# Kernel tuning notes

Measured on AMD Instinct MI355X. Metric: run time of the kernel, lower is better.

## Reference

```python
import jax, jax.numpy as jnp
import numpy as np

OUT_F, IN_F = 11008, 4096
GROUP = 64                      # group_size, axis=0 grouping
G = OUT_F * IN_F // GROUP       # number of groups = 704512


def setup_inputs() -> dict:
    key = jax.random.key(0)
    ks = jax.random.split(key, 7)
    x = jax.random.normal(ks[0], (512, IN_F), dtype=jnp.float32)
    # packed 4-bit weights: two nibbles per byte, packed along the group axis
    W_q = jax.random.randint(ks[1], (GROUP // 2, G), 0, 256, dtype=jnp.int32)
    # per-group dequant params (scale = 1/quant_scale in the torch code)
    scale = jax.random.uniform(ks[2], (1, G), dtype=jnp.float32) * 0.01 + 1e-4
    zero = jax.random.uniform(ks[3], (1, G), dtype=jnp.float32) * 15.0
    # low-rank correction (LoRC): W_eff = W_dq + U @ V
    U = jax.random.normal(ks[4], (OUT_F, 32), dtype=jnp.float32) * 0.02
    V = jax.random.normal(ks[5], (32, IN_F), dtype=jnp.float32) * 0.02
    bias = jax.random.normal(ks[6], (OUT_F,), dtype=jnp.float32)
    return {"x": x, "W_q": W_q, "scale": scale, "zero": zero,
            "U": U, "V": V, "bias": bias}


def _dequantize(W_q, scale, zero):
    # unpack_4bit_u8: high nibble -> first half of rows, low nibble -> second half
    hi = ((W_q >> 4) & 0xF).astype(jnp.float32)   # [32, G]
    lo = (W_q & 0xF).astype(jnp.float32)          # [32, G]
    Wg = jnp.concatenate([hi, lo], axis=0)        # [64, G] = [group_size, G]
    W = (Wg - zero) * scale                       # per-group affine dequant
    return W.reshape(OUT_F, IN_F)


def reference(x, W_q, scale, zero, U, V, bias):
    W = _dequantize(W_q, scale, zero)             # [out, in]
    W = W + U @ V                                 # low-rank correction
    # nn.Linear semantics: out = x @ W.T + bias
    return x @ W.T + bias
```

## Files before the change

kernel.cpp:

```cpp
#include <hip/hip_runtime.h>
#include <cstdint>

typedef short  s16x8 __attribute__((ext_vector_type(8)));
typedef float  f32x4 __attribute__((ext_vector_type(4)));
typedef int    i32x4 __attribute__((ext_vector_type(4)));
typedef int    i32x2 __attribute__((ext_vector_type(2)));
typedef unsigned short u16x4 __attribute__((ext_vector_type(4)));

#define OUT_F 11008
#define IN_F  4096
#define MROWS 512
#define GQ4   176128
#define HALF  5504
#define RMOD  172

__device__ __forceinline__ unsigned short f2bf(float f) {
  unsigned u = __builtin_bit_cast(unsigned, f);
  return (unsigned short)((u + 0x8000u) >> 16);
}
__device__ __forceinline__ float bfbits(unsigned bits) {
  return __builtin_bit_cast(float, bits);
}
__device__ __forceinline__ unsigned cvtpk(float a, float b) {
  unsigned r;
  asm("v_cvt_pk_bf16_f32 %0, %1, %2" : "=v"(r) : "v"(a), "v"(b));
  return r;
}

__global__ __launch_bounds__(256) void convert_k(const float* __restrict__ x,
                                                 const float* __restrict__ U,
                                                 unsigned short* __restrict__ xbf,
                                                 unsigned short* __restrict__ Ubf) {
  int i = blockIdx.x * 256 + threadIdx.x;
  const int NX = (MROWS * IN_F) / 4;
  const int NU = (OUT_F * 32) / 4;
  if (i >= NX + NU) return;
  const float* src; unsigned short* dst; int idx;
  if (i < NX) { src = x; dst = xbf; idx = i; }
  else        { src = U; dst = Ubf; idx = i - NX; }
  f32x4 v = *(const f32x4*)(src + (size_t)idx * 4);
  u16x4 o;
  o[0] = f2bf(v[0]); o[1] = f2bf(v[1]); o[2] = f2bf(v[2]); o[3] = f2bf(v[3]);
  *(u16x4*)(dst + (size_t)idx * 4) = o;
}

__global__ __launch_bounds__(256) void mz_k(const float* __restrict__ scale,
                                            const float* __restrict__ zero,
                                            f32x4* __restrict__ mz) {
  int idx = blockIdx.x * 256 + threadIdx.x;
  if (idx >= 176128) return;
  f32x4 s = *(const f32x4*)(scale + (size_t)idx * 4);
  f32x4 z = *(const f32x4*)(zero  + (size_t)idx * 4);
  f32x4 m;
#pragma unroll
  for (int e = 0; e < 4; ++e) m[e] = -(z[e] + 128.f) * s[e];
  mz[idx] = m;
}

__global__ __launch_bounds__(256) void pcalc_k(const float* __restrict__ x,
                                               const float* __restrict__ V,
                                               float* __restrict__ P) {
  int m  = (blockIdx.x >> 3) * 8 + (threadIdx.x >> 5);
  int j  = threadIdx.x & 31;
  int k0 = (blockIdx.x & 7) * 512;
  const float* xr = x + (size_t)m * IN_F + k0;
  const float* vr = V + (size_t)j * IN_F + k0;
  float a = 0.f;
#pragma unroll 4
  for (int k = 0; k < 512; k += 4) {
    f32x4 xv = *(const f32x4*)(xr + k);
    f32x4 vv = *(const f32x4*)(vr + k);
    a += xv[0]*vv[0] + xv[1]*vv[1] + xv[2]*vv[2] + xv[3]*vv[3];
  }
  atomicAdd(P + m * 32 + j, a);
}

__global__ __launch_bounds__(256) void wdeq_k(const i32x4* __restrict__ Wq4,
                                              const float* __restrict__ scale,
                                              const float* __restrict__ zero,
                                              unsigned short* __restrict__ Wbf) {
  int n  = blockIdx.x * 256 + threadIdx.x;
  int jo = n / 88064;
  int ch = n - jo * 88064;
  int r  = ch >> 9;
  const int chL = ch & 511;
  const int cc0 = ch * 8;
  f32x4 s0 = *(const f32x4*)(scale + cc0);
  f32x4 s1 = *(const f32x4*)(scale + cc0 + 4);
  f32x4 z0 = *(const f32x4*)(zero + cc0);
  f32x4 z1 = *(const f32x4*)(zero + cc0 + 4);
  float sv[8], mzv[8];
#pragma unroll
  for (int e = 0; e < 4; ++e) {
    sv[e]      = s0[e]; mzv[e]     = -(z0[e] + 128.f) * s0[e];
    sv[e + 4]  = s1[e]; mzv[e + 4] = -(z1[e] + 128.f) * s1[e];
  }
#pragma unroll
  for (int jj = 0; jj < 8; ++jj) {
    int j = jo * 8 + jj;
    i32x4 w0 = Wq4[(size_t)j * GQ4 + ch * 2];
    i32x4 w1 = Wq4[(size_t)j * GQ4 + ch * 2 + 1];
    float h[8], l[8];
#pragma unroll
    for (int e = 0; e < 8; ++e) {
      int v = (e < 4) ? w0[e] : w1[e - 4];
      float qh = bfbits(0x43000000u | (((unsigned)v & 0xF0u) << 12));
      float ql = bfbits(0x43000000u | (((unsigned)v & 0x0Fu) << 16));
      h[e] = __builtin_fmaf(qh, sv[e], mzv[e]);
      l[e] = __builtin_fmaf(ql, sv[e], mzv[e]);
    }
    i32x4 hh = { (int)cvtpk(h[0], h[1]), (int)cvtpk(h[2], h[3]),
                 (int)cvtpk(h[4], h[5]), (int)cvtpk(h[6], h[7]) };
    i32x4 ll = { (int)cvtpk(l[0], l[1]), (int)cvtpk(l[2], l[3]),
                 (int)cvtpk(l[4], l[5]), (int)cvtpk(l[6], l[7]) };
    int o  = j * RMOD + r;
    int o2 = o + HALF;
    unsigned sc  = ((unsigned)chL & ~7u) | (((unsigned)chL ^ (unsigned)o)  & 7u);
    unsigned sc2 = ((unsigned)chL & ~7u) | (((unsigned)chL ^ (unsigned)o2) & 7u);
    *(i32x4*)(Wbf + (size_t)o  * IN_F + sc  * 8) = hh;
    *(i32x4*)(Wbf + (size_t)o2 * IN_F + sc2 * 8) = ll;
  }
}

__global__ __launch_bounds__(512, 6) void gemm_fast(
    const unsigned short* __restrict__ xbf,
    const unsigned short* __restrict__ Wbf,
    const float*          __restrict__ Pf,
    const i32x4*          __restrict__ Ubf4,
    const float*          __restrict__ bias,
    float*                __restrict__ out)
{
  extern __shared__ __align__(16) unsigned short smem[];

  const int tid  = threadIdx.x;
  const int lane = tid & 63;
  const int wid  = tid >> 6;
  const int wm   = wid >> 2;
  const int wn   = wid & 3;

  const int b  = blockIdx.x;
  const int L  = (b & 7) * 86 + (b >> 3);
  const int gn = L >> 3;
  const int gm = L & 7;
  const int m0 = gm * 64;
  const int o0 = gn * 128;

  const int arow = tid >> 3;
  const unsigned a_src = (unsigned)(m0 + arow) * IN_F +
                         (((tid & 7) ^ (arow & 7)) * 8);
  size_t b_src[2];
#pragma unroll
  for (int it = 0; it < 2; ++it)
    b_src[it] = (size_t)(o0 + it * 64 + (tid >> 3)) * IN_F + (tid & 7) * 8;

  const int akey   = (lane & 7) << 3;
  const int a_base = (wm * 32 + (lane & 15)) * 64 + ((lane >> 4) * 8);
  const int b_base = (wn * 32 + (lane & 15)) * 64 + ((lane >> 4) * 8);

  f32x4 acc[2][2];
  {
    f32x4 zf = {0.f, 0.f, 0.f, 0.f};
#pragma unroll
    for (int i = 0; i < 2; ++i)
#pragma unroll
      for (int j = 0; j < 2; ++j) acc[i][j] = zf;
  }
  f32x4 pf0, pf1; i32x4 uuF;

  auto issueA = [&](int buf, int k0s) {
    unsigned short* Adst = smem + buf * 4096;
    __builtin_amdgcn_global_load_lds(
        (const __attribute__((address_space(1))) unsigned int*)(xbf + a_src + k0s),
        (__attribute__((address_space(3))) unsigned int*)(Adst + tid * 8),
        16, 0, 0);
  };
  auto issueB = [&](int buf, int k0s) {
    unsigned short* Bdst = smem + 8192 + buf * 8192;
#pragma unroll
    for (int it = 0; it < 2; ++it) {
      __builtin_amdgcn_global_load_lds(
          (const __attribute__((address_space(1))) unsigned int*)(Wbf + b_src[it] + k0s),
          (__attribute__((address_space(3))) unsigned int*)(Bdst + it * 4096 + tid * 8),
          16, 0, 0);
    }
  };
  auto compute = [&](int buf) {
    const unsigned short* Ac = smem + buf * 4096;
    const unsigned short* Bc = smem + 8192 + buf * 8192;
    __builtin_amdgcn_s_setprio(1);
#pragma unroll
    for (int kk = 0; kk < 64; kk += 32) {
      s16x8 av[2], bv[2];
#pragma unroll
      for (int f = 0; f < 2; ++f)
        av[f] = *(const s16x8*)(Ac + ((a_base + f * 1024 + kk) ^ akey));
#pragma unroll
      for (int f = 0; f < 2; ++f)
        bv[f] = *(const s16x8*)(Bc + ((b_base + f * 1024 + kk) ^ akey));
#pragma unroll
      for (int i = 0; i < 2; ++i)
#pragma unroll
        for (int j = 0; j < 2; ++j)
          acc[i][j] = __builtin_amdgcn_mfma_f32_16x16x32_bf16(av[i], bv[j], acc[i][j], 0, 0, 0);
    }
    __builtin_amdgcn_s_setprio(0);
  };
  auto loadF = [&]() {
    int row = tid >> 3, h8 = tid & 7;
    if (h8 < 4) {
      pf0 = *(const f32x4*)(Pf + (m0 + row) * 32 + h8 * 8);
      pf1 = *(const f32x4*)(Pf + (m0 + row) * 32 + h8 * 8 + 4);
    }
    int rw = tid >> 2, h4 = tid & 3;
    uuF = Ubf4[(size_t)(o0 + rw) * 4 + h4];
  };
  auto writeF = [&](int buf) {
    unsigned short* An = smem + buf * 4096;
    unsigned short* Bn = smem + 8192 + buf * 8192;
    i32x4 zi = {0, 0, 0, 0};
    {
      int row = tid >> 3, h8 = tid & 7, key = row & 7;
      i32x4 v = zi;
      if (h8 < 4)
        v = i32x4{ (int)cvtpk(pf0[0], pf0[1]), (int)cvtpk(pf0[2], pf0[3]),
                   (int)cvtpk(pf1[0], pf1[1]), (int)cvtpk(pf1[2], pf1[3]) };
      *(i32x4*)(An + row * 64 + ((h8 ^ key) * 8)) = v;
    }
    {
      int rw = tid >> 2, h4 = tid & 3, key = rw & 7;
      *(i32x4*)(Bn + rw * 64 + ((h4 ^ key) * 8))       = uuF;
      *(i32x4*)(Bn + rw * 64 + (((h4 + 4) ^ key) * 8)) = zi;
    }
  };

  issueA(0, 0);
  issueB(0, 0);
  __syncthreads();

  for (int t = 0; t < 63; ++t) {
    int cur = t & 1, nxt = cur ^ 1;
    issueA(nxt, (t + 1) * 64);
    issueB(nxt, (t + 1) * 64);
    compute(cur);
    __syncthreads();
  }
  loadF();
  compute(1);
  writeF(0);
  __syncthreads();
  compute(0);

#pragma unroll
  for (int fn = 0; fn < 2; ++fn) {
    int o = o0 + wn * 32 + fn * 16 + (lane & 15);
    float bv = bias[o];
#pragma unroll
    for (int fm = 0; fm < 2; ++fm) {
      int m = m0 + wm * 32 + fm * 16 + ((lane >> 4) << 2);
#pragma unroll
      for (int j = 0; j < 4; ++j)
        out[(size_t)(m + j) * OUT_F + o] = acc[fm][fn][j] + bv;
    }
  }
}

__global__ __launch_bounds__(512, 6) void milo_gemm(
    const unsigned short* __restrict__ xbf,
    const i32x4*          __restrict__ Wq4,
    const f32x4*          __restrict__ Sc4,
    const f32x4*          __restrict__ Mz4,
    const float*          __restrict__ Pf,
    const i32x4*          __restrict__ Ubf4,
    const float*          __restrict__ bias,
    float*                __restrict__ out)
{
  extern __shared__ __align__(16) unsigned short smem[];
  const int tid  = threadIdx.x;
  const int lane = tid & 63;
  const int wid  = tid >> 6;
  const int wm   = wid >> 1;
  const int wn   = wid & 1;
  const int b  = blockIdx.x;
  const int L  = (b & 7) * 86 + (b >> 3);
  const int gn = L >> 2;
  const int gm = L & 3;
  const int m0 = gm * 128;
  const int o0 = gn * 32;
  const int tr = tid >> 4;
  unsigned wq_off, sc_off;
  {
    int o = o0 + tr;
    int g = o / RMOD;
    int r = o - g * RMOD;
    wq_off = (unsigned)g * GQ4 + (unsigned)r * 1024u + (tid & 15);
    sc_off = (unsigned)r * 1024u + (tid & 15);
  }
  unsigned a_src[2];
#pragma unroll
  for (int it = 0; it < 2; ++it) {
    int row   = wid * 16 + it * 8 + (lane >> 3);
    int chunk = (lane & 7) ^ (lane >> 3);
    a_src[it] = (unsigned)(m0 + row) * IN_F + chunk * 8;
  }
  const int akey   = (lane & 7) << 3;
  const int a_base = (wm * 32 + (lane & 15)) * 64 + ((lane >> 4) * 8);
  const int b_base = (wn * 32 + (lane & 15)) * 64 + ((lane >> 4) * 8);
  f32x4 acc[2][2];
  {
    f32x4 zf = {0.f, 0.f, 0.f, 0.f};
#pragma unroll
    for (int i = 0; i < 2; ++i)
#pragma unroll
      for (int j = 0; j < 2; ++j) acc[i][j] = zf;
  }
  i32x4 wq; f32x4 s4, mz4;
  f32x4 pf[2]; i32x4 uuF;
  auto issueA = [&](int buf, int k0s) {
    unsigned short* Adst = smem + buf * 8192;
#pragma unroll
    for (int it = 0; it < 2; ++it) {
      __builtin_amdgcn_global_load_lds(
          (const __attribute__((address_space(1))) unsigned int*)(xbf + a_src[it] + k0s),
          (__attribute__((address_space(3))) unsigned int*)(Adst + (wid * 16 + it * 8) * 64),
          16, 0, 0);
    }
  };
  auto loadB = [&](int kq) {
    wq  = Wq4[wq_off + kq];
    s4  = Sc4[sc_off + kq];
    mz4 = Mz4[sc_off + kq];
  };
  auto writeB = [&](int buf) {
    unsigned short* Bn = smem + 16384 + buf * 4096;
    int scol = ((tid & 15) * 4) ^ ((tr & 7) << 3);
    float h[4], l[4];
#pragma unroll
    for (int e = 0; e < 4; ++e) {
      int v = wq[e];
      float qh = bfbits(0x43000000u | (((unsigned)v & 0xF0u) << 12));
      float ql = bfbits(0x43000000u | (((unsigned)v & 0x0Fu) << 16));
      h[e] = __builtin_fmaf(qh, s4[e], mz4[e]);
      l[e] = __builtin_fmaf(ql, s4[e], mz4[e]);
    }
    i32x2 hh = { (int)cvtpk(h[0], h[1]), (int)cvtpk(h[2], h[3]) };
    i32x2 ll = { (int)cvtpk(l[0], l[1]), (int)cvtpk(l[2], l[3]) };
    *(i32x2*)(Bn + tr * 64 + scol)        = hh;
    *(i32x2*)(Bn + (tr + 32) * 64 + scol) = ll;
  };
  auto loadF = [&]() {
    int row = tid >> 2, h4 = tid & 3;
#pragma unroll
    for (int q = 0; q < 2; ++q)
      pf[q] = *(const f32x4*)(Pf + (m0 + row) * 32 + h4 * 8 + q * 4);
    int rw = tid >> 3, h8 = tid & 7;
    int oc = (rw < 32) ? (o0 + rw) : (HALF + o0 + rw - 32);
    uuF = Ubf4[oc * 4 + (h8 & 3)];
  };
  auto writeF = [&](int buf) {
    unsigned short* An = smem + buf * 8192;
    unsigned short* Bn = smem + 16384 + buf * 4096;
    i32x4 zi = {0, 0, 0, 0};
    {
      int row = tid >> 2, h4 = tid & 3;
      int key = (row & 7) << 3;
      i32x4 t4 = { (int)cvtpk(pf[0][0], pf[0][1]), (int)cvtpk(pf[0][2], pf[0][3]),
                   (int)cvtpk(pf[1][0], pf[1][1]), (int)cvtpk(pf[1][2], pf[1][3]) };
      *(i32x4*)(An + row * 64 + ((h4 * 8) ^ key))      = t4;
      *(i32x4*)(An + row * 64 + ((32 + h4 * 8) ^ key)) = zi;
    }
    {
      int rw = tid >> 3, h8 = tid & 7;
      int key = (rw & 7) << 3;
      *(i32x4*)(Bn + rw * 64 + ((h8 * 8) ^ key)) = (h8 < 4) ? uuF : zi;
    }
  };
  auto compute = [&](int buf) {
    const unsigned short* Ac = smem + buf * 8192;
    const unsigned short* Bc = smem + 16384 + buf * 4096;
    __builtin_amdgcn_s_setprio(1);
#pragma unroll
    for (int kk = 0; kk < 64; kk += 32) {
      s16x8 av[2], bv[2];
#pragma unroll
      for (int f = 0; f < 2; ++f)
        av[f] = *(const s16x8*)(Ac + ((a_base + f * 1024 + kk) ^ akey));
#pragma unroll
      for (int f = 0; f < 2; ++f)
        bv[f] = *(const s16x8*)(Bc + ((b_base + f * 1024 + kk) ^ akey));
#pragma unroll
      for (int i = 0; i < 2; ++i)
#pragma unroll
        for (int j = 0; j < 2; ++j)
          acc[i][j] = __builtin_amdgcn_mfma_f32_16x16x32_bf16(av[i], bv[j], acc[i][j], 0, 0, 0);
    }
    __builtin_amdgcn_s_setprio(0);
  };
  loadB(0);
  issueA(0, 0);
  writeB(0);
  __syncthreads();
  for (int t = 0; t < 63; ++t) {
    int cur = t & 1, nxt = cur ^ 1;
    loadB((t + 1) * 16);
    issueA(nxt, (t + 1) * 64);
    compute(cur);
    writeB(nxt);
    __syncthreads();
  }
  loadF();
  compute(1);
  writeF(0);
  __syncthreads();
  compute(0);
#pragma unroll
  for (int fn = 0; fn < 2; ++fn) {
    int c = wn * 32 + fn * 16 + (lane & 15);
    int o = (c < 32) ? (o0 + c) : (HALF + o0 + (c - 32));
    float bv = bias[o];
#pragma unroll
    for (int fm = 0; fm < 2; ++fm) {
      int m = m0 + wm * 32 + fm * 16 + ((lane >> 4) << 2);
#pragma unroll
      for (int j = 0; j < 4; ++j)
        out[(size_t)(m + j) * OUT_F + o] = acc[fm][fn][j] + bv;
    }
  }
}

extern "C" void kernel_launch(void* const* d_in, const int* in_sizes, int n_in,
                              void* d_out, int out_size, void* d_ws, size_t ws_size,
                              hipStream_t stream) {
  const float* x     = (const float*)d_in[0];
  const int*   Wq    = (const int*)d_in[1];
  const float* scale = (const float*)d_in[2];
  const float* zero  = (const float*)d_in[3];
  const float* U     = (const float*)d_in[4];
  const float* V     = (const float*)d_in[5];
  const float* bias  = (const float*)d_in[6];
  float* out = (float*)d_out;

  unsigned short* xbf = (unsigned short*)d_ws;
  unsigned short* Ubf = xbf + (size_t)MROWS * IN_F;
  float*          P   = (float*)(Ubf + (size_t)OUT_F * 32);
  char*           rest = (char*)(P + (size_t)MROWS * 32);
  const size_t base   = (size_t)MROWS * IN_F * 2 + (size_t)OUT_F * 32 * 2
                      + (size_t)MROWS * 32 * 4;
  const size_t wbf_sz = (size_t)OUT_F * IN_F * 2;

  (void)hipMemsetAsync(P, 0, (size_t)MROWS * 32 * sizeof(float), stream);
  convert_k<<<2392, 256, 0, stream>>>(x, U, xbf, Ubf);
  pcalc_k<<<512, 256, 0, stream>>>(x, V, P);

  if (ws_size >= base + wbf_sz) {
    unsigned short* Wbf = (unsigned short*)rest;
    wdeq_k<<<1376, 256, 0, stream>>>((const i32x4*)Wq, scale, zero, Wbf);
    gemm_fast<<<688, 512, 49152, stream>>>(xbf, Wbf, P, (const i32x4*)Ubf,
                                           bias, out);
  } else {
    float* mz = (float*)rest;
    mz_k<<<688, 256, 0, stream>>>(scale, zero, (f32x4*)mz);
    milo_gemm<<<688, 512, 49152, stream>>>(xbf, (const i32x4*)Wq,
                                           (const f32x4*)scale, (const f32x4*)mz,
                                           P, (const i32x4*)Ubf, bias, out);
  }
}
```

Baseline: 137.3 us.

## Double GEMM M-tile to 128 rows and flatten dequant kernel parallelism

The bf16 GEMM block tile grows from 64x128 to 128x128. Each wave now holds 4x2 MFMA accumulators, the grid halves to 344 blocks, shared memory rises to 64 KB, and launch bounds drop to 4 blocks per CU. The goal is to cut redundant W tile reloads from global memory by reusing each B tile across more rows of x. The dequant kernel also drops its 8-iteration loop over j and launches 8x more threads, one output chunk each, for more parallelism in exchange for reloading scale and zero once per thread. The trade-off is that 344 blocks may underfill the GPU's CUs and the larger tile raises register pressure.

```diff
diff --git a/kernel.cpp b/kernel.cpp
--- a/kernel.cpp
+++ b/kernel.cpp
@@ -79,50 +79,43 @@
                                               const float* __restrict__ scale,
                                               const float* __restrict__ zero,
                                               unsigned short* __restrict__ Wbf) {
-  int n  = blockIdx.x * 256 + threadIdx.x;
-  int jo = n / 88064;
-  int ch = n - jo * 88064;
-  int r  = ch >> 9;
-  const int chL = ch & 511;
+  int n   = blockIdx.x * 256 + threadIdx.x;
+  int j   = n / 88064;
+  int ch  = n - j * 88064;
+  int r   = ch >> 9;
+  int chL = ch & 511;
   const int cc0 = ch * 8;
   f32x4 s0 = *(const f32x4*)(scale + cc0);
   f32x4 s1 = *(const f32x4*)(scale + cc0 + 4);
   f32x4 z0 = *(const f32x4*)(zero + cc0);
   f32x4 z1 = *(const f32x4*)(zero + cc0 + 4);
-  float sv[8], mzv[8];
-#pragma unroll
-  for (int e = 0; e < 4; ++e) {
-    sv[e]      = s0[e]; mzv[e]     = -(z0[e] + 128.f) * s0[e];
-    sv[e + 4]  = s1[e]; mzv[e + 4] = -(z1[e] + 128.f) * s1[e];
-  }
-#pragma unroll
-  for (int jj = 0; jj < 8; ++jj) {
-    int j = jo * 8 + jj;
-    i32x4 w0 = Wq4[(size_t)j * GQ4 + ch * 2];
-    i32x4 w1 = Wq4[(size_t)j * GQ4 + ch * 2 + 1];
-    float h[8], l[8];
-#pragma unroll
-    for (int e = 0; e < 8; ++e) {
-      int v = (e < 4) ? w0[e] : w1[e - 4];
-      float qh = bfbits(0x43000000u | (((unsigned)v & 0xF0u) << 12));
-      float ql = bfbits(0x43000000u | (((unsigned)v & 0x0Fu) << 16));
-      h[e] = __builtin_fmaf(qh, sv[e], mzv[e]);
-      l[e] = __builtin_fmaf(ql, sv[e], mzv[e]);
-    }
-    i32x4 hh = { (int)cvtpk(h[0], h[1]), (int)cvtpk(h[2], h[3]),
-                 (int)cvtpk(h[4], h[5]), (int)cvtpk(h[6], h[7]) };
-    i32x4 ll = { (int)cvtpk(l[0], l[1]), (int)cvtpk(l[2], l[3]),
-                 (int)cvtpk(l[4], l[5]), (int)cvtpk(l[6], l[7]) };
-    int o  = j * RMOD + r;
-    int o2 = o + HALF;
-    unsigned sc  = ((unsigned)chL & ~7u) | (((unsigned)chL ^ (unsigned)o)  & 7u);
-    unsigned sc2 = ((unsigned)chL & ~7u) | (((unsigned)chL ^ (unsigned)o2) & 7u);
-    *(i32x4*)(Wbf + (size_t)o  * IN_F + sc  * 8) = hh;
-    *(i32x4*)(Wbf + (size_t)o2 * IN_F + sc2 * 8) = ll;
-  }
-}
-
-__global__ __launch_bounds__(512, 6) void gemm_fast(
+  i32x4 w0 = Wq4[(size_t)j * GQ4 + ch * 2];
+  i32x4 w1 = Wq4[(size_t)j * GQ4 + ch * 2 + 1];
+  float h[8], l[8];
+#pragma unroll
+  for (int e = 0; e < 8; ++e) {
+    int   v = (e < 4) ? w0[e] : w1[e - 4];
+    float s = (e < 4) ? s0[e] : s1[e - 4];
+    float z = (e < 4) ? z0[e] : z1[e - 4];
+    float m = -(z + 128.f) * s;
+    float qh = bfbits(0x43000000u | (((unsigned)v & 0xF0u) << 12));
+    float ql = bfbits(0x43000000u | (((unsigned)v & 0x0Fu) << 16));
+    h[e] = __builtin_fmaf(qh, s, m);
+    l[e] = __builtin_fmaf(ql, s, m);
+  }
+  i32x4 hh = { (int)cvtpk(h[0], h[1]), (int)cvtpk(h[2], h[3]),
+               (int)cvtpk(h[4], h[5]), (int)cvtpk(h[6], h[7]) };
+  i32x4 ll = { (int)cvtpk(l[0], l[1]), (int)cvtpk(l[2], l[3]),
+               (int)cvtpk(l[4], l[5]), (int)cvtpk(l[6], l[7]) };
+  int o  = j * RMOD + r;
+  int o2 = o + HALF;
+  unsigned sc  = ((unsigned)chL & ~7u) | (((unsigned)chL ^ (unsigned)o)  & 7u);
+  unsigned sc2 = ((unsigned)chL & ~7u) | (((unsigned)chL ^ (unsigned)o2) & 7u);
+  *(i32x4*)(Wbf + (size_t)o  * IN_F + sc  * 8) = hh;
+  *(i32x4*)(Wbf + (size_t)o2 * IN_F + sc2 * 8) = ll;
+}
+
+__global__ __launch_bounds__(512, 4) void gemm_fast(
     const unsigned short* __restrict__ xbf,
     const unsigned short* __restrict__ Wbf,
     const float*          __restrict__ Pf,
@@ -139,43 +132,48 @@
   const int wn   = wid & 3;
 
   const int b  = blockIdx.x;
-  const int L  = (b & 7) * 86 + (b >> 3);
-  const int gn = L >> 3;
-  const int gm = L & 7;
-  const int m0 = gm * 64;
+  const int L  = (b & 7) * 43 + (b >> 3);
+  const int gn = L >> 2;
+  const int gm = L & 3;
+  const int m0 = gm * 128;
   const int o0 = gn * 128;
 
-  const int arow = tid >> 3;
-  const unsigned a_src = (unsigned)(m0 + arow) * IN_F +
-                         (((tid & 7) ^ (arow & 7)) * 8);
+  unsigned a_src[2];
+#pragma unroll
+  for (int it = 0; it < 2; ++it)
+    a_src[it] = (unsigned)(m0 + it * 64 + (tid >> 3)) * IN_F +
+                (((tid & 7) ^ ((tid >> 3) & 7)) * 8);
   size_t b_src[2];
 #pragma unroll
   for (int it = 0; it < 2; ++it)
     b_src[it] = (size_t)(o0 + it * 64 + (tid >> 3)) * IN_F + (tid & 7) * 8;
 
   const int akey   = (lane & 7) << 3;
-  const int a_base = (wm * 32 + (lane & 15)) * 64 + ((lane >> 4) * 8);
+  const int a_base = (wm * 64 + (lane & 15)) * 64 + ((lane >> 4) * 8);
   const int b_base = (wn * 32 + (lane & 15)) * 64 + ((lane >> 4) * 8);
 
-  f32x4 acc[2][2];
+  f32x4 acc[4][2];
   {
     f32x4 zf = {0.f, 0.f, 0.f, 0.f};
 #pragma unroll
-    for (int i = 0; i < 2; ++i)
+    for (int i = 0; i < 4; ++i)
 #pragma unroll
       for (int j = 0; j < 2; ++j) acc[i][j] = zf;
   }
   f32x4 pf0, pf1; i32x4 uuF;
 
   auto issueA = [&](int buf, int k0s) {
-    unsigned short* Adst = smem + buf * 4096;
-    __builtin_amdgcn_global_load_lds(
-        (const __attribute__((address_space(1))) unsigned int*)(xbf + a_src + k0s),
-        (__attribute__((address_space(3))) unsigned int*)(Adst + tid * 8),
-        16, 0, 0);
+    unsigned short* Adst = smem + buf * 8192;
+#pragma unroll
+    for (int it = 0; it < 2; ++it) {
+      __builtin_amdgcn_global_load_lds(
+          (const __attribute__((address_space(1))) unsigned int*)(xbf + a_src[it] + k0s),
+          (__attribute__((address_space(3))) unsigned int*)(Adst + it * 4096 + tid * 8),
+          16, 0, 0);
+    }
   };
   auto issueB = [&](int buf, int k0s) {
-    unsigned short* Bdst = smem + 8192 + buf * 8192;
+    unsigned short* Bdst = smem + 16384 + buf * 8192;
 #pragma unroll
     for (int it = 0; it < 2; ++it) {
       __builtin_amdgcn_global_load_lds(
@@ -185,20 +183,20 @@
     }
   };
   auto compute = [&](int buf) {
-    const unsigned short* Ac = smem + buf * 4096;
-    const unsigned short* Bc = smem + 8192 + buf * 8192;
+    const unsigned short* Ac = smem + buf * 8192;
+    const unsigned short* Bc = smem + 16384 + buf * 8192;
     __builtin_amdgcn_s_setprio(1);
 #pragma unroll
     for (int kk = 0; kk < 64; kk += 32) {
-      s16x8 av[2], bv[2];
-#pragma unroll
-      for (int f = 0; f < 2; ++f)
+      s16x8 av[4], bv[2];
+#pragma unroll
+      for (int f = 0; f < 4; ++f)
         av[f] = *(const s16x8*)(Ac + ((a_base + f * 1024 + kk) ^ akey));
 #pragma unroll
       for (int f = 0; f < 2; ++f)
         bv[f] = *(const s16x8*)(Bc + ((b_base + f * 1024 + kk) ^ akey));
 #pragma unroll
-      for (int i = 0; i < 2; ++i)
+      for (int i = 0; i < 4; ++i)
 #pragma unroll
         for (int j = 0; j < 2; ++j)
           acc[i][j] = __builtin_amdgcn_mfma_f32_16x16x32_bf16(av[i], bv[j], acc[i][j], 0, 0, 0);
@@ -206,31 +204,22 @@
     __builtin_amdgcn_s_setprio(0);
   };
   auto loadF = [&]() {
-    int row = tid >> 3, h8 = tid & 7;
-    if (h8 < 4) {
-      pf0 = *(const f32x4*)(Pf + (m0 + row) * 32 + h8 * 8);
-      pf1 = *(const f32x4*)(Pf + (m0 + row) * 32 + h8 * 8 + 4);
-    }
-    int rw = tid >> 2, h4 = tid & 3;
-    uuF = Ubf4[(size_t)(o0 + rw) * 4 + h4];
+    int row = tid >> 2, h4 = tid & 3;
+    pf0 = *(const f32x4*)(Pf + (m0 + row) * 32 + h4 * 8);
+    pf1 = *(const f32x4*)(Pf + (m0 + row) * 32 + h4 * 8 + 4);
+    uuF = Ubf4[(size_t)(o0 + row) * 4 + h4];
   };
   auto writeF = [&](int buf) {
-    unsigned short* An = smem + buf * 4096;
-    unsigned short* Bn = smem + 8192 + buf * 8192;
+    unsigned short* An = smem + buf * 8192;
+    unsigned short* Bn = smem + 16384 + buf * 8192;
     i32x4 zi = {0, 0, 0, 0};
-    {
-      int row = tid >> 3, h8 = tid & 7, key = row & 7;
-      i32x4 v = zi;
-      if (h8 < 4)
-        v = i32x4{ (int)cvtpk(pf0[0], pf0[1]), (int)cvtpk(pf0[2], pf0[3]),
-                   (int)cvtpk(pf1[0], pf1[1]), (int)cvtpk(pf1[2], pf1[3]) };
-      *(i32x4*)(An + row * 64 + ((h8 ^ key) * 8)) = v;
-    }
-    {
-      int rw = tid >> 2, h4 = tid & 3, key = rw & 7;
-      *(i32x4*)(Bn + rw * 64 + ((h4 ^ key) * 8))       = uuF;
-      *(i32x4*)(Bn + rw * 64 + (((h4 + 4) ^ key) * 8)) = zi;
-    }
+    int row = tid >> 2, h4 = tid & 3, key = row & 7;
+    i32x4 t4 = { (int)cvtpk(pf0[0], pf0[1]), (int)cvtpk(pf0[2], pf0[3]),
+                 (int)cvtpk(pf1[0], pf1[1]), (int)cvtpk(pf1[2], pf1[3]) };
+    *(i32x4*)(An + row * 64 + ((h4 ^ key) * 8))       = t4;
+    *(i32x4*)(An + row * 64 + (((h4 + 4) ^ key) * 8)) = zi;
+    *(i32x4*)(Bn + row * 64 + ((h4 ^ key) * 8))       = uuF;
+    *(i32x4*)(Bn + row * 64 + (((h4 + 4) ^ key) * 8)) = zi;
   };
 
   issueA(0, 0);
@@ -255,8 +244,8 @@
     int o = o0 + wn * 32 + fn * 16 + (lane & 15);
     float bv = bias[o];
 #pragma unroll
-    for (int fm = 0; fm < 2; ++fm) {
-      int m = m0 + wm * 32 + fm * 16 + ((lane >> 4) << 2);
+    for (int fm = 0; fm < 4; ++fm) {
+      int m = m0 + wm * 64 + fm * 16 + ((lane >> 4) << 2);
 #pragma unroll
       for (int j = 0; j < 4; ++j)
         out[(size_t)(m + j) * OUT_F + o] = acc[fm][fn][j] + bv;
@@ -453,8 +442,8 @@
 
   if (ws_size >= base + wbf_sz) {
     unsigned short* Wbf = (unsigned short*)rest;
-    wdeq_k<<<1376, 256, 0, stream>>>((const i32x4*)Wq, scale, zero, Wbf);
-    gemm_fast<<<688, 512, 49152, stream>>>(xbf, Wbf, P, (const i32x4*)Ubf,
+    wdeq_k<<<11008, 256, 0, stream>>>((const i32x4*)Wq, scale, zero, Wbf);
+    gemm_fast<<<344, 512, 65536, stream>>>(xbf, Wbf, P, (const i32x4*)Ubf,
                                            bias, out);
   } else {
     float* mz = (float*)rest;
```

New measurement: 132.5 us. -3.5%, faster.

## Fuse prep kernels into one launch and triple-buffer the bf16 GEMM pipeline

Applied to the files above, without the earlier changes.

Merges the weight dequantization, x/U bf16 conversion and x@V projection into a single prep kernel, with one 4-bit group slice per thread instead of eight per thread. This removes two launches and lets the three preprocessing jobs overlap on the device. The GEMM switches from double to triple buffering in LDS, using explicit vmcnt waits and raw barriers so loads run two stages ahead. LDS per block grows to 72KB and the occupancy hint drops from 6 to 4, which may reduce the number of resident blocks.

```diff
diff --git a/kernel.cpp b/kernel.cpp
--- a/kernel.cpp
+++ b/kernel.cpp
@@ -25,6 +25,237 @@
   unsigned r;
   asm("v_cvt_pk_bf16_f32 %0, %1, %2" : "=v"(r) : "v"(a), "v"(b));
   return r;
+}
+
+__global__ __launch_bounds__(256) void prep_k(const float* __restrict__ x,
+                                              const float* __restrict__ U,
+                                              const float* __restrict__ scale,
+                                              const float* __restrict__ zero,
+                                              const float* __restrict__ V,
+                                              const i32x4* __restrict__ Wq4,
+                                              unsigned short* __restrict__ xbf,
+                                              unsigned short* __restrict__ Ubf,
+                                              float* __restrict__ P,
+                                              unsigned short* __restrict__ Wbf) {
+  const int blk = blockIdx.x;
+  const int tid = threadIdx.x;
+  if (blk < 11008) {
+    int n   = blk * 256 + tid;
+    int j   = n / 88064;
+    int ch  = n - j * 88064;
+    int r   = ch >> 9;
+    int chL = ch & 511;
+    const int cc0 = ch * 8;
+    f32x4 s0 = *(const f32x4*)(scale + cc0);
+    f32x4 s1 = *(const f32x4*)(scale + cc0 + 4);
+    f32x4 z0 = *(const f32x4*)(zero + cc0);
+    f32x4 z1 = *(const f32x4*)(zero + cc0 + 4);
+    i32x4 w0 = Wq4[(size_t)j * GQ4 + ch * 2];
+    i32x4 w1 = Wq4[(size_t)j * GQ4 + ch * 2 + 1];
+    float h[8], l[8];
+#pragma unroll
+    for (int e = 0; e < 8; ++e) {
+      int   v = (e < 4) ? w0[e] : w1[e - 4];
+      float s = (e < 4) ? s0[e] : s1[e - 4];
+      float z = (e < 4) ? z0[e] : z1[e - 4];
+      float m = -(z + 128.f) * s;
+      float qh = bfbits(0x43000000u | (((unsigned)v & 0xF0u) << 12));
+      float ql = bfbits(0x43000000u | (((unsigned)v & 0x0Fu) << 16));
+      h[e] = __builtin_fmaf(qh, s, m);
+      l[e] = __builtin_fmaf(ql, s, m);
+    }
+    i32x4 hh = { (int)cvtpk(h[0], h[1]), (int)cvtpk(h[2], h[3]),
+                 (int)cvtpk(h[4], h[5]), (int)cvtpk(h[6], h[7]) };
+    i32x4 ll = { (int)cvtpk(l[0], l[1]), (int)cvtpk(l[2], l[3]),
+                 (int)cvtpk(l[4], l[5]), (int)cvtpk(l[6], l[7]) };
+    int o  = j * RMOD + r;
+    int o2 = o + HALF;
+    unsigned sc  = ((unsigned)chL & ~7u) | (((unsigned)chL ^ (unsigned)o)  & 7u);
+    unsigned sc2 = ((unsigned)chL & ~7u) | (((unsigned)chL ^ (unsigned)o2) & 7u);
+    *(i32x4*)(Wbf + (size_t)o  * IN_F + sc  * 8) = hh;
+    *(i32x4*)(Wbf + (size_t)o2 * IN_F + sc2 * 8) = ll;
+  } else if (blk < 13400) {
+    int i = (blk - 11008) * 256 + tid;
+    const int NX = (MROWS * IN_F) / 4;
+    const int NU = (OUT_F * 32) / 4;
+    if (i >= NX + NU) return;
+    const float* src; unsigned short* dst; int idx;
+    if (i < NX) { src = x; dst = xbf; idx = i; }
+    else        { src = U; dst = Ubf; idx = i - NX; }
+    f32x4 v = *(const f32x4*)(src + (size_t)idx * 4);
+    u16x4 o;
+    o[0] = f2bf(v[0]); o[1] = f2bf(v[1]); o[2] = f2bf(v[2]); o[3] = f2bf(v[3]);
+    *(u16x4*)(dst + (size_t)idx * 4) = o;
+  } else {
+    int bp = blk - 13400;
+    int m  = (bp >> 3) * 8 + (tid >> 5);
+    int j  = tid & 31;
+    int k0 = (bp & 7) * 512;
+    const float* xr = x + (size_t)m * IN_F + k0;
+    const float* vr = V + (size_t)j * IN_F + k0;
+    float a = 0.f;
+#pragma unroll 4
+    for (int k = 0; k < 512; k += 4) {
+      f32x4 xv = *(const f32x4*)(xr + k);
+      f32x4 vv = *(const f32x4*)(vr + k);
+      a += xv[0]*vv[0] + xv[1]*vv[1] + xv[2]*vv[2] + xv[3]*vv[3];
+    }
+    atomicAdd(P + m * 32 + j, a);
+  }
+}
+
+__global__ __launch_bounds__(512, 4) void gemm_fast(
+    const unsigned short* __restrict__ xbf,
+    const unsigned short* __restrict__ Wbf,
+    const float*          __restrict__ Pf,
+    const i32x4*          __restrict__ Ubf4,
+    const float*          __restrict__ bias,
+    float*                __restrict__ out)
+{
+  extern __shared__ __align__(16) unsigned short smem[];
+
+  const int tid  = threadIdx.x;
+  const int lane = tid & 63;
+  const int wid  = tid >> 6;
+  const int wm   = wid >> 2;
+  const int wn   = wid & 3;
+
+  const int b  = blockIdx.x;
+  const int L  = (b & 7) * 86 + (b >> 3);
+  const int gn = L >> 3;
+  const int gm = L & 7;
+  const int m0 = gm * 64;
+  const int o0 = gn * 128;
+
+  const int arow = tid >> 3;
+  const unsigned a_src = (unsigned)(m0 + arow) * IN_F +
+                         (((tid & 7) ^ (arow & 7)) * 8);
+  size_t b_src[2];
+#pragma unroll
+  for (int it = 0; it < 2; ++it)
+    b_src[it] = (size_t)(o0 + it * 64 + (tid >> 3)) * IN_F + (tid & 7) * 8;
+
+  const int akey   = (lane & 7) << 3;
+  const int a_base = (wm * 32 + (lane & 15)) * 64 + ((lane >> 4) * 8);
+  const int b_base = (wn * 32 + (lane & 15)) * 64 + ((lane >> 4) * 8);
+
+  f32x4 acc[2][2];
+  {
+    f32x4 zf = {0.f, 0.f, 0.f, 0.f};
+#pragma unroll
+    for (int i = 0; i < 2; ++i)
+#pragma unroll
+      for (int j = 0; j < 2; ++j) acc[i][j] = zf;
+  }
+  f32x4 pf0, pf1; i32x4 uuF;
+
+  auto issueT = [&](int ring, int k0s) {
+    unsigned short* Adst = smem + ring * 4096;
+    unsigned short* Bdst = smem + 12288 + ring * 8192;
+    __builtin_amdgcn_global_load_lds(
+        (const __attribute__((address_space(1))) unsigned int*)(xbf + a_src + k0s),
+        (__attribute__((address_space(3))) unsigned int*)(Adst + tid * 8),
+        16, 0, 0);
+#pragma unroll
+    for (int it = 0; it < 2; ++it) {
+      __builtin_amdgcn_global_load_lds(
+          (const __attribute__((address_space(1))) unsigned int*)(Wbf + b_src[it] + k0s),
+          (__attribute__((address_space(3))) unsigned int*)(Bdst + it * 4096 + tid * 8),
+          16, 0, 0);
+    }
+  };
+  auto compute = [&](int ring) {
+    const unsigned short* Ac = smem + ring * 4096;
+    const unsigned short* Bc = smem + 12288 + ring * 8192;
+    __builtin_amdgcn_s_setprio(1);
+#pragma unroll
+    for (int kk = 0; kk < 64; kk += 32) {
+      s16x8 av[2], bv[2];
+#pragma unroll
+      for (int f = 0; f < 2; ++f)
+        av[f] = *(const s16x8*)(Ac + ((a_base + f * 1024 + kk) ^ akey));
+#pragma unroll
+      for (int f = 0; f < 2; ++f)
+        bv[f] = *(const s16x8*)(Bc + ((b_base + f * 1024 + kk) ^ akey));
+#pragma unroll
+      for (int i = 0; i < 2; ++i)
+#pragma unroll
+        for (int j = 0; j < 2; ++j)
+          acc[i][j] = __builtin_amdgcn_mfma_f32_16x16x32_bf16(av[i], bv[j], acc[i][j], 0, 0, 0);
+    }
+    __builtin_amdgcn_s_setprio(0);
+  };
+  auto loadF = [&]() {
+    int row = tid >> 3, h8 = tid & 7;
+    if (h8 < 4) {
+      pf0 = *(const f32x4*)(Pf + (m0 + row) * 32 + h8 * 8);
+      pf1 = *(const f32x4*)(Pf + (m0 + row) * 32 + h8 * 8 + 4);
+    }
+    int rw = tid >> 2, h4 = tid & 3;
+    uuF = Ubf4[(size_t)(o0 + rw) * 4 + h4];
+  };
+  auto writeF = [&](int ring) {
+    unsigned short* An = smem + ring * 4096;
+    unsigned short* Bn = smem + 12288 + ring * 8192;
+    i32x4 zi = {0, 0, 0, 0};
+    {
+      int row = tid >> 3, h8 = tid & 7, key = row & 7;
+      i32x4 v = zi;
+      if (h8 < 4)
+        v = i32x4{ (int)cvtpk(pf0[0], pf0[1]), (int)cvtpk(pf0[2], pf0[3]),
+                   (int)cvtpk(pf1[0], pf1[1]), (int)cvtpk(pf1[2], pf1[3]) };
+      *(i32x4*)(An + row * 64 + ((h8 ^ key) * 8)) = v;
+    }
+    {
+      int rw = tid >> 2, h4 = tid & 3, key = rw & 7;
+      *(i32x4*)(Bn + rw * 64 + ((h4 ^ key) * 8))       = uuF;
+      *(i32x4*)(Bn + rw * 64 + (((h4 + 4) ^ key) * 8)) = zi;
+    }
+  };
+
+#define WAIT_LGKM0 asm volatile("s_waitcnt lgkmcnt(0)" ::: "memory")
+#define WAIT_VM(N) asm volatile("s_waitcnt vmcnt(" #N ")" ::: "memory")
+#define BAR        __builtin_amdgcn_s_barrier()
+
+  issueT(0, 0);
+  issueT(1, 64);
+  WAIT_VM(3);
+  BAR;
+
+#define STEP(RB, TI, IB) \
+  issueT(IB, (TI) * 64); compute(RB); WAIT_LGKM0; WAIT_VM(3); BAR;
+
+  for (int t3 = 0; t3 < 60; t3 += 3) {
+    STEP(0, t3 + 2, 2)
+    STEP(1, t3 + 3, 0)
+    STEP(2, t3 + 4, 1)
+  }
+  STEP(0, 62, 2)
+  STEP(1, 63, 0)
+  compute(2); WAIT_LGKM0; WAIT_VM(0); BAR;
+  loadF();
+  compute(0);
+  writeF(1);
+  WAIT_LGKM0; BAR;
+  compute(1);
+
+#undef STEP
+#undef WAIT_LGKM0
+#undef WAIT_VM
+#undef BAR
+
+#pragma unroll
+  for (int fn = 0; fn < 2; ++fn) {
+    int o = o0 + wn * 32 + fn * 16 + (lane & 15);
+    float bv = bias[o];
+#pragma unroll
+    for (int fm = 0; fm < 2; ++fm) {
+      int m = m0 + wm * 32 + fm * 16 + ((lane >> 4) << 2);
+#pragma unroll
+      for (int j = 0; j < 4; ++j)
+        out[(size_t)(m + j) * OUT_F + o] = acc[fm][fn][j] + bv;
+    }
+  }
 }
 
 __global__ __launch_bounds__(256) void convert_k(const float* __restrict__ x,
@@ -73,195 +304,6 @@
     a += xv[0]*vv[0] + xv[1]*vv[1] + xv[2]*vv[2] + xv[3]*vv[3];
   }
   atomicAdd(P + m * 32 + j, a);
-}
-
-__global__ __launch_bounds__(256) void wdeq_k(const i32x4* __restrict__ Wq4,
-                                              const float* __restrict__ scale,
-                                              const float* __restrict__ zero,
-                                              unsigned short* __restrict__ Wbf) {
-  int n  = blockIdx.x * 256 + threadIdx.x;
-  int jo = n / 88064;
-  int ch = n - jo * 88064;
-  int r  = ch >> 9;
-  const int chL = ch & 511;
-  const int cc0 = ch * 8;
-  f32x4 s0 = *(const f32x4*)(scale + cc0);
-  f32x4 s1 = *(const f32x4*)(scale + cc0 + 4);
-  f32x4 z0 = *(const f32x4*)(zero + cc0);
-  f32x4 z1 = *(const f32x4*)(zero + cc0 + 4);
-  float sv[8], mzv[8];
-#pragma unroll
-  for (int e = 0; e < 4; ++e) {
-    sv[e]      = s0[e]; mzv[e]     = -(z0[e] + 128.f) * s0[e];
-    sv[e + 4]  = s1[e]; mzv[e + 4] = -(z1[e] + 128.f) * s1[e];
-  }
-#pragma unroll
-  for (int jj = 0; jj < 8; ++jj) {
-    int j = jo * 8 + jj;
-    i32x4 w0 = Wq4[(size_t)j * GQ4 + ch * 2];
-    i32x4 w1 = Wq4[(size_t)j * GQ4 + ch * 2 + 1];
-    float h[8], l[8];
-#pragma unroll
-    for (int e = 0; e < 8; ++e) {
-      int v = (e < 4) ? w0[e] : w1[e - 4];
-      float qh = bfbits(0x43000000u | (((unsigned)v & 0xF0u) << 12));
-      float ql = bfbits(0x43000000u | (((unsigned)v & 0x0Fu) << 16));
-      h[e] = __builtin_fmaf(qh, sv[e], mzv[e]);
-      l[e] = __builtin_fmaf(ql, sv[e], mzv[e]);
-    }
-    i32x4 hh = { (int)cvtpk(h[0], h[1]), (int)cvtpk(h[2], h[3]),
-                 (int)cvtpk(h[4], h[5]), (int)cvtpk(h[6], h[7]) };
-    i32x4 ll = { (int)cvtpk(l[0], l[1]), (int)cvtpk(l[2], l[3]),
-                 (int)cvtpk(l[4], l[5]), (int)cvtpk(l[6], l[7]) };
-    int o  = j * RMOD + r;
-    int o2 = o + HALF;
-    unsigned sc  = ((unsigned)chL & ~7u) | (((unsigned)chL ^ (unsigned)o)  & 7u);
-    unsigned sc2 = ((unsigned)chL & ~7u) | (((unsigned)chL ^ (unsigned)o2) & 7u);
-    *(i32x4*)(Wbf + (size_t)o  * IN_F + sc  * 8) = hh;
-    *(i32x4*)(Wbf + (size_t)o2 * IN_F + sc2 * 8) = ll;
-  }
-}
-
-__global__ __launch_bounds__(512, 6) void gemm_fast(
-    const unsigned short* __restrict__ xbf,
-    const unsigned short* __restrict__ Wbf,
-    const float*          __restrict__ Pf,
-    const i32x4*          __restrict__ Ubf4,
-    const float*          __restrict__ bias,
-    float*                __restrict__ out)
-{
-  extern __shared__ __align__(16) unsigned short smem[];
-
-  const int tid  = threadIdx.x;
-  const int lane = tid & 63;
-  const int wid  = tid >> 6;
-  const int wm   = wid >> 2;
-  const int wn   = wid & 3;
-
-  const int b  = blockIdx.x;
-  const int L  = (b & 7) * 86 + (b >> 3);
-  const int gn = L >> 3;
-  const int gm = L & 7;
-  const int m0 = gm * 64;
-  const int o0 = gn * 128;
-
-  const int arow = tid >> 3;
-  const unsigned a_src = (unsigned)(m0 + arow) * IN_F +
-                         (((tid & 7) ^ (arow & 7)) * 8);
-  size_t b_src[2];
-#pragma unroll
-  for (int it = 0; it < 2; ++it)
-    b_src[it] = (size_t)(o0 + it * 64 + (tid >> 3)) * IN_F + (tid & 7) * 8;
-
-  const int akey   = (lane & 7) << 3;
-  const int a_base = (wm * 32 + (lane & 15)) * 64 + ((lane >> 4) * 8);
-  const int b_base = (wn * 32 + (lane & 15)) * 64 + ((lane >> 4) * 8);
-
-  f32x4 acc[2][2];
-  {
-    f32x4 zf = {0.f, 0.f, 0.f, 0.f};
-#pragma unroll
-    for (int i = 0; i < 2; ++i)
-#pragma unroll
-      for (int j = 0; j < 2; ++j) acc[i][j] = zf;
-  }
-  f32x4 pf0, pf1; i32x4 uuF;
-
-  auto issueA = [&](int buf, int k0s) {
-    unsigned short* Adst = smem + buf * 4096;
-    __builtin_amdgcn_global_load_lds(
-        (const __attribute__((address_space(1))) unsigned int*)(xbf + a_src + k0s),
-        (__attribute__((address_space(3))) unsigned int*)(Adst + tid * 8),
-        16, 0, 0);
-  };
-  auto issueB = [&](int buf, int k0s) {
-    unsigned short* Bdst = smem + 8192 + buf * 8192;
-#pragma unroll
-    for (int it = 0; it < 2; ++it) {
-      __builtin_amdgcn_global_load_lds(
-          (const __attribute__((address_space(1))) unsigned int*)(Wbf + b_src[it] + k0s),
-          (__attribute__((address_space(3))) unsigned int*)(Bdst + it * 4096 + tid * 8),
-          16, 0, 0);
-    }
-  };
-  auto compute = [&](int buf) {
-    const unsigned short* Ac = smem + buf * 4096;
-    const unsigned short* Bc = smem + 8192 + buf * 8192;
-    __builtin_amdgcn_s_setprio(1);
-#pragma unroll
-    for (int kk = 0; kk < 64; kk += 32) {
-      s16x8 av[2], bv[2];
-#pragma unroll
-      for (int f = 0; f < 2; ++f)
-        av[f] = *(const s16x8*)(Ac + ((a_base + f * 1024 + kk) ^ akey));
-#pragma unroll
-      for (int f = 0; f < 2; ++f)
-        bv[f] = *(const s16x8*)(Bc + ((b_base + f * 1024 + kk) ^ akey));
-#pragma unroll
-      for (int i = 0; i < 2; ++i)
-#pragma unroll
-        for (int j = 0; j < 2; ++j)
-          acc[i][j] = __builtin_amdgcn_mfma_f32_16x16x32_bf16(av[i], bv[j], acc[i][j], 0, 0, 0);
-    }
-    __builtin_amdgcn_s_setprio(0);
-  };
-  auto loadF = [&]() {
-    int row = tid >> 3, h8 = tid & 7;
-    if (h8 < 4) {
-      pf0 = *(const f32x4*)(Pf + (m0 + row) * 32 + h8 * 8);
-      pf1 = *(const f32x4*)(Pf + (m0 + row) * 32 + h8 * 8 + 4);
-    }
-    int rw = tid >> 2, h4 = tid & 3;
-    uuF = Ubf4[(size_t)(o0 + rw) * 4 + h4];
-  };
-  auto writeF = [&](int buf) {
-    unsigned short* An = smem + buf * 4096;
-    unsigned short* Bn = smem + 8192 + buf * 8192;
-    i32x4 zi = {0, 0, 0, 0};
-    {
-      int row = tid >> 3, h8 = tid & 7, key = row & 7;
-      i32x4 v = zi;
-      if (h8 < 4)
-        v = i32x4{ (int)cvtpk(pf0[0], pf0[1]), (int)cvtpk(pf0[2], pf0[3]),
-                   (int)cvtpk(pf1[0], pf1[1]), (int)cvtpk(pf1[2], pf1[3]) };
-      *(i32x4*)(An + row * 64 + ((h8 ^ key) * 8)) = v;
-    }
-    {
-      int rw = tid >> 2, h4 = tid & 3, key = rw & 7;
-      *(i32x4*)(Bn + rw * 64 + ((h4 ^ key) * 8))       = uuF;
-      *(i32x4*)(Bn + rw * 64 + (((h4 + 4) ^ key) * 8)) = zi;
-    }
-  };
-
-  issueA(0, 0);
-  issueB(0, 0);
-  __syncthreads();
-
-  for (int t = 0; t < 63; ++t) {
-    int cur = t & 1, nxt = cur ^ 1;
-    issueA(nxt, (t + 1) * 64);
-    issueB(nxt, (t + 1) * 64);
-    compute(cur);
-    __syncthreads();
-  }
-  loadF();
-  compute(1);
-  writeF(0);
-  __syncthreads();
-  compute(0);
-
-#pragma unroll
-  for (int fn = 0; fn < 2; ++fn) {
-    int o = o0 + wn * 32 + fn * 16 + (lane & 15);
-    float bv = bias[o];
-#pragma unroll
-    for (int fm = 0; fm < 2; ++fm) {
-      int m = m0 + wm * 32 + fm * 16 + ((lane >> 4) << 2);
-#pragma unroll
-      for (int j = 0; j < 4; ++j)
-        out[(size_t)(m + j) * OUT_F + o] = acc[fm][fn][j] + bv;
-    }
-  }
 }
 
 __global__ __launch_bounds__(512, 6) void milo_gemm(
@@ -448,16 +490,17 @@
   const size_t wbf_sz = (size_t)OUT_F * IN_F * 2;
 
   (void)hipMemsetAsync(P, 0, (size_t)MROWS * 32 * sizeof(float), stream);
-  convert_k<<<2392, 256, 0, stream>>>(x, U, xbf, Ubf);
-  pcalc_k<<<512, 256, 0, stream>>>(x, V, P);
 
   if (ws_size >= base + wbf_sz) {
     unsigned short* Wbf = (unsigned short*)rest;
-    wdeq_k<<<1376, 256, 0, stream>>>((const i32x4*)Wq, scale, zero, Wbf);
-    gemm_fast<<<688, 512, 49152, stream>>>(xbf, Wbf, P, (const i32x4*)Ubf,
+    prep_k<<<13912, 256, 0, stream>>>(x, U, scale, zero, V, (const i32x4*)Wq,
+                                      xbf, Ubf, P, Wbf);
+    gemm_fast<<<688, 512, 73728, stream>>>(xbf, Wbf, P, (const i32x4*)Ubf,
                                            bias, out);
   } else {
     float* mz = (float*)rest;
+    convert_k<<<2392, 256, 0, stream>>>(x, U, xbf, Ubf);
+    pcalc_k<<<512, 256, 0, stream>>>(x, V, P);
     mz_k<<<688, 256, 0, stream>>>(scale, zero, (f32x4*)mz);
     milo_gemm<<<688, 512, 49152, stream>>>(xbf, (const i32x4*)Wq,
                                            (const f32x4*)scale, (const f32x4*)mz,
```

Result: slower. 217.7 us (+58.6%).
